# Kernel tuning notes

Measured on AMD Instinct MI355X. Metric: run time of the kernel, lower is better.

## Reference

```python
import jax, jax.numpy as jnp
import numpy as np

BS, EP = 32, 32
N_AGENTS, N_ATOM, EMBED = 8, 51, 32
STATE_DIM, HYP = 128, 64
V_MIN, V_MAX = -10.0, 10.0


def proj(support, probs, v_min, v_max, n_atom):
    # C51 categorical projection of (support, probs) onto the fixed atom grid
    # linspace(v_min, v_max, n_atom). support/probs: [..., M] -> [..., n_atom]
    support, probs = jnp.broadcast_arrays(support, probs)
    delta = (v_max - v_min) / (n_atom - 1)
    b = (jnp.clip(support, v_min, v_max) - v_min) / delta
    l = jnp.floor(b)
    u = jnp.ceil(b)
    eq = (u == l).astype(probs.dtype)  # support exactly on an atom -> all mass to l
    ml = probs * (u - b + eq)
    mu = probs * (b - l)
    shp = probs.shape
    n = int(np.prod(shp[:-1]))
    m = shp[-1]
    rows = jnp.arange(n)[:, None]
    out = jnp.zeros((n, n_atom), probs.dtype)
    out = out.at[rows, l.astype(jnp.int32).reshape(n, m)].add(ml.reshape(n, m))
    out = out.at[rows, u.astype(jnp.int32).reshape(n, m)].add(mu.reshape(n, m))
    return out.reshape(shp[:-1] + (n_atom,))


def bconv(p, q):
    # Full 1D convolution of per-row categorical pmfs (sum of two random vars).
    # p: [N, L], q: [N, M] -> [N, L+M-1], via grouped conv (one group per row).
    N, L = p.shape
    M = q.shape[-1]
    out = jax.lax.conv_general_dilated(
        p[None], jnp.flip(q, -1)[:, None, :],
        window_strides=(1,), padding=[(M - 1, M - 1)],
        feature_group_count=N, dimension_numbers=('NCW', 'OIW', 'NCW'))
    return out[0]


def mlp2(x, w1, b1, w2, b2):
    return jax.nn.relu(x @ w1.T + b1) @ w2.T + b2


def setup_inputs():
    key = jax.random.key(0)
    ks = jax.random.split(key, 20)
    def p(k, shape, s=0.05):
        return jax.random.normal(k, shape, dtype=jnp.float32) * s
    aq = jax.random.uniform(ks[0], (BS, EP, N_AGENTS, N_ATOM), dtype=jnp.float32)
    aq = aq / jnp.sum(aq, -1, keepdims=True)  # valid categorical distributions
    return {
        'agent_qs_distri': aq,
        'states': p(ks[1], (BS, EP, STATE_DIM), 1.0),
        'hw1_w1': p(ks[2], (HYP, STATE_DIM)), 'hw1_b1': p(ks[3], (HYP,)),
        'hw1_w2': p(ks[4], (EMBED * N_AGENTS, HYP)), 'hw1_b2': p(ks[5], (EMBED * N_AGENTS,)),
        'hb1_w': p(ks[6], (EMBED, STATE_DIM)), 'hb1_b': p(ks[7], (EMBED,)),
        'hwf_w1': p(ks[8], (HYP, STATE_DIM)), 'hwf_b1': p(ks[9], (HYP,)),
        'hwf_w2': p(ks[10], (EMBED, HYP)), 'hwf_b2': p(ks[11], (EMBED,)),
        'v_w1': p(ks[12], (EMBED, STATE_DIM)), 'v_b1': p(ks[13], (EMBED,)),
        'v_w2': p(ks[14], (1, EMBED)), 'v_b2': p(ks[15], (1,)),
    }


def reference(agent_qs_distri, states, hw1_w1, hw1_b1, hw1_w2, hw1_b2,
              hb1_w, hb1_b, hwf_w1, hwf_b1, hwf_w2, hwf_b2,
              v_w1, v_b1, v_w2, v_b2):
    bs, ep, n_agents, n_atom = agent_qs_distri.shape
    s = states.reshape(-1, STATE_DIM)
    atoms = jnp.linspace(V_MIN, V_MAX, n_atom).astype(jnp.float32)  # [A]

    w1 = jnp.abs(mlp2(s, hw1_w1, hw1_b1, hw1_w2, hw1_b2)).reshape(bs, ep, EMBED, n_agents)
    b1 = (s @ hb1_w.T + hb1_b).reshape(bs, ep, EMBED)

    # stage 1: scale each agent's support by w1[..., k, i], project back onto atoms
    sup1 = atoms * w1[..., None]                                       # [bs,ep,E,Na,A]
    aw = proj(sup1, agent_qs_distri[:, :, None], V_MIN, V_MAX, n_atom)  # [bs,ep,E,Na,A]
    awf = aw.reshape(-1, n_agents, n_atom)                              # [bs*ep*E,Na,A]
    q = awf[:, 0]
    for i in range(1, n_agents):
        q = bconv(q, awf[:, i])                                         # [.., Na*A-Na+1]
    L1 = n_agents * n_atom - n_agents + 1
    sup = jnp.linspace(n_agents * V_MIN, n_agents * V_MAX, L1).astype(jnp.float32)
    sup = jax.nn.elu(sup + b1[..., None])                               # [bs,ep,E,L1]
    x = proj(sup, q.reshape(bs, ep, EMBED, L1), V_MIN, V_MAX, n_atom)   # [bs,ep,E,A]

    # stage 2: hyper_w_final scaling, convolve across embed dim, add V(s)
    wf = jnp.abs(mlp2(s, hwf_w1, hwf_b1, hwf_w2, hwf_b2)).reshape(bs, ep, EMBED)
    xw = proj(atoms * wf[..., None], x, V_MIN, V_MAX, n_atom)           # [bs,ep,E,A]
    xwf = xw.reshape(-1, EMBED, n_atom)
    q = xwf[:, 0]
    for i in range(1, EMBED):
        q = bconv(q, xwf[:, i])                                         # [bs*ep, E*A-E+1]
    L2 = EMBED * n_atom - EMBED + 1
    v = mlp2(s, v_w1, v_b1, v_w2, v_b2).reshape(bs, ep, 1)
    sup2 = jnp.linspace(EMBED * V_MIN, EMBED * V_MAX, L2).astype(jnp.float32) + v
    return proj(sup2, q.reshape(bs, ep, L2), V_MIN, V_MAX, n_atom)      # [bs,ep,A]
```

## Files before the change

kernel.cpp:

```cpp
#include <hip/hip_runtime.h>
#include <hip/hip_bf16.h>
#include <math.h>

typedef unsigned short u16;

#define WAVE_SYNC() asm volatile("s_waitcnt lgkmcnt(0)" ::: "memory")

__device__ __forceinline__ float bf2f(u16 u) {
  union { unsigned int i; float f; } c;
  c.i = ((unsigned int)u) << 16;
  return c.f;
}
__device__ __forceinline__ float bflo(unsigned int u) {
  union { unsigned int i; float f; } c; c.i = u << 16; return c.f;
}
__device__ __forceinline__ float bfhi(unsigned int u) {
  union { unsigned int i; float f; } c; c.i = u & 0xffff0000u; return c.f;
}
__device__ __forceinline__ u16 f2bf(float f) {
  union { float f; unsigned int i; } c;
  c.f = f;
  unsigned int x = c.i;
  unsigned int r = (x + 0x7fffu + ((x >> 16) & 1u)) >> 16;
  return (u16)r;
}

__device__ __forceinline__ void proj_bounds(float wv, int& ML, int& MH) {
  float smin = (-10.0f + 0.4f * 0.0f)  * wv;
  float smax = (-10.0f + 0.4f * 50.0f) * wv;
  float bmin = (fminf(fmaxf(smin, -10.0f), 10.0f) + 10.0f) / 0.4f;
  float bmax = (fminf(fmaxf(smax, -10.0f), 10.0f) + 10.0f) / 0.4f;
  ML = (int)floorf(bmin);
  MH = (int)ceilf(bmax);
}

__device__ __forceinline__ void conv_pad2(const float* __restrict__ q,
                                          float* __restrict__ qn,
                                          const float* __restrict__ kvs,
                                          int ML, int W, int T,
                                          int LQ, int HQ, int tid, int nthr)
{
  const int Lout = LQ + ML, Hout = HQ + ML + T;
  for (int J = Lout + tid; J <= Hout; J += nthr) {
    const float* qp = q + (J - ML);
    float acc = 0.f;
    for (int c = 0; c < W; c += 4) {
      float4 k4 = *(const float4*)(kvs + c);
      acc = fmaf(k4.x, qp[-c],     acc);
      acc = fmaf(k4.y, qp[-c - 1], acc);
      acc = fmaf(k4.z, qp[-c - 2], acc);
      acc = fmaf(k4.w, qp[-c - 3], acc);
    }
    qn[J] = acc;
  }
}

__device__ __forceinline__ void conv16(const float* __restrict__ q,
                                       float* __restrict__ qn,
                                       const float* __restrict__ kvs,
                                       int ML, int T,
                                       int LQ, int HQ, int tid, int nthr)
{
  const int Lout = LQ + ML, Hout = HQ + ML + T;
  for (int J = Lout + tid; J <= Hout; J += nthr) {
    const float* qp = q + (J - ML);
    float a0 = 0.f, a1 = 0.f;
#pragma unroll
    for (int c = 0; c < 16; c += 4) {
      float4 k4 = *(const float4*)(kvs + c);
      a0 = fmaf(k4.x, qp[-c],     a0);
      a1 = fmaf(k4.y, qp[-c - 1], a1);
      a0 = fmaf(k4.z, qp[-c - 2], a0);
      a1 = fmaf(k4.w, qp[-c - 3], a1);
    }
    qn[J] = a0 + a1;
  }
}

__device__ __forceinline__ void conv8(const float* __restrict__ q,
                                      float* __restrict__ qn,
                                      const float* __restrict__ kvs,
                                      int ML, int T,
                                      int LQ, int HQ, int tid, int nthr)
{
  const int Lout = LQ + ML, Hout = HQ + ML + T;
  for (int J = Lout + tid; J <= Hout; J += nthr) {
    const float* qp = q + (J - ML);
    float a0 = 0.f, a1 = 0.f;
#pragma unroll
    for (int c = 0; c < 8; c += 4) {
      float4 k4 = *(const float4*)(kvs + c);
      a0 = fmaf(k4.x, qp[-c],     a0);
      a1 = fmaf(k4.y, qp[-c - 1], a1);
      a0 = fmaf(k4.z, qp[-c - 2], a0);
      a1 = fmaf(k4.w, qp[-c - 3], a1);
    }
    qn[J] = a0 + a1;
  }
}

template<int TA, int TB>
__device__ __forceinline__ float gather_part(const float* __restrict__ pb,
                                             float wv, float j)
{
  float a0 = 0.f, a1 = 0.f, a2 = 0.f, a3 = 0.f;
  const float4* pb4 = (const float4*)pb;
  const float base = 25.0f - j;
#pragma unroll
  for (int t4 = TA; t4 < TB; ++t4) {
    float4 p4 = pb4[t4];
#define G1(PX, TT, AC) { \
    float sup = ((float)(TT) * 0.4f - 10.0f) * wv; \
    float c   = fminf(fmaxf(sup, -10.0f), 10.0f); \
    float d   = fmaf(c, 2.5f, base); \
    AC = fmaf(PX, fmaxf(0.f, 1.0f - fabsf(d)), AC); }
    G1(p4.x, 4 * t4 + 0, a0)
    G1(p4.y, 4 * t4 + 1, a1)
    G1(p4.z, 4 * t4 + 2, a2)
    G1(p4.w, 4 * t4 + 3, a3)
#undef G1
  }
  return (a0 + a1) + (a2 + a3);
}

template<int BF>
__device__ __forceinline__ float ldt(const void* p, int i) {
  if (BF) return bf2f(((const u16*)p)[i]);
  return ((const float*)p)[i];
}

template<int BF>
__device__ __forceinline__ float dot128_t(const void* w, int row, const float* s) {
  float acc = 0.f;
  if (BF) {
    const uint4* p = (const uint4*)((const u16*)w + row * 128);
#pragma unroll
    for (int i = 0; i < 16; ++i) {
      uint4 v = p[i];
      int b = i * 8;
      acc = fmaf(bflo(v.x), s[b + 0], acc); acc = fmaf(bfhi(v.x), s[b + 1], acc);
      acc = fmaf(bflo(v.y), s[b + 2], acc); acc = fmaf(bfhi(v.y), s[b + 3], acc);
      acc = fmaf(bflo(v.z), s[b + 4], acc); acc = fmaf(bfhi(v.z), s[b + 5], acc);
      acc = fmaf(bflo(v.w), s[b + 6], acc); acc = fmaf(bfhi(v.w), s[b + 7], acc);
    }
  } else {
    const float4* p = (const float4*)((const float*)w + row * 128);
#pragma unroll
    for (int i = 0; i < 32; ++i) {
      float4 v = p[i];
      int b = i * 4;
      acc = fmaf(v.x, s[b + 0], acc); acc = fmaf(v.y, s[b + 1], acc);
      acc = fmaf(v.z, s[b + 2], acc); acc = fmaf(v.w, s[b + 3], acc);
    }
  }
  return acc;
}

template<int BF>
__device__ __forceinline__ float dot64_t(const void* w, int row, const float* h) {
  float acc = 0.f;
  if (BF) {
    const uint4* p = (const uint4*)((const u16*)w + row * 64);
#pragma unroll
    for (int i = 0; i < 8; ++i) {
      uint4 v = p[i];
      int b = i * 8;
      acc = fmaf(bflo(v.x), h[b + 0], acc); acc = fmaf(bfhi(v.x), h[b + 1], acc);
      acc = fmaf(bflo(v.y), h[b + 2], acc); acc = fmaf(bfhi(v.y), h[b + 3], acc);
      acc = fmaf(bflo(v.z), h[b + 4], acc); acc = fmaf(bfhi(v.z), h[b + 5], acc);
      acc = fmaf(bflo(v.w), h[b + 6], acc); acc = fmaf(bfhi(v.w), h[b + 7], acc);
    }
  } else {
    const float4* p = (const float4*)((const float*)w + row * 64);
#pragma unroll
    for (int i = 0; i < 16; ++i) {
      float4 v = p[i];
      int b = i * 4;
      acc = fmaf(v.x, h[b + 0], acc); acc = fmaf(v.y, h[b + 1], acc);
      acc = fmaf(v.z, h[b + 2], acc); acc = fmaf(v.w, h[b + 3], acc);
    }
  }
  return acc;
}

template<int BF>
__device__ __forceinline__ void mlp_par(
    const void* states,
    const void* hw1_w1, const void* hw1_b1, const void* hw1_w2, const void* hw1_b2,
    const void* hb1_w,  const void* hb1_b,
    const void* hwf_w1, const void* hwf_b1, const void* hwf_w2, const void* hwf_b2,
    const void* v_w1,   const void* v_b1,   const void* v_w2,   const void* v_b2,
    float* w1_ws, float* b1_ws, float* wf_ws, float* v_ws,
    float* s_st, float* h1, float* hf, float* vh, int n, int tid)
{
  if (tid < 128) s_st[tid] = ldt<BF>(states, n * 128 + tid);
  __syncthreads();
  if (tid < 64)
    h1[tid] = fmaxf(dot128_t<BF>(hw1_w1, tid, s_st) + ldt<BF>(hw1_b1, tid), 0.f);
  else if (tid < 128)
    hf[tid - 64] = fmaxf(dot128_t<BF>(hwf_w1, tid - 64, s_st) + ldt<BF>(hwf_b1, tid - 64), 0.f);
  else if (tid < 160)
    vh[tid - 128] = fmaxf(dot128_t<BF>(v_w1, tid - 128, s_st) + ldt<BF>(v_b1, tid - 128), 0.f);
  else if (tid < 192)
    b1_ws[n * 32 + tid - 160] = dot128_t<BF>(hb1_w, tid - 160, s_st) + ldt<BF>(hb1_b, tid - 160);
  __syncthreads();
  if (tid < 256)
    w1_ws[n * 256 + tid] = fabsf(dot64_t<BF>(hw1_w2, tid, h1) + ldt<BF>(hw1_b2, tid));
  else if (tid < 288)
    wf_ws[n * 32 + tid - 256] = fabsf(dot64_t<BF>(hwf_w2, tid - 256, hf) + ldt<BF>(hwf_b2, tid - 256));
  else {
    int l2 = tid - 288;
    float part = vh[l2] * ldt<BF>(v_w2, l2);
    part += __shfl_xor(part, 1);  part += __shfl_xor(part, 2);
    part += __shfl_xor(part, 4);  part += __shfl_xor(part, 8);
    part += __shfl_xor(part, 16);
    if (l2 == 0) v_ws[n] = part + ldt<BF>(v_b2, 0);
  }
}

__global__ __launch_bounds__(320) void k_mlp(
    const void* __restrict__ states,
    const void* __restrict__ hw1_w1, const void* __restrict__ hw1_b1,
    const void* __restrict__ hw1_w2, const void* __restrict__ hw1_b2,
    const void* __restrict__ hb1_w,  const void* __restrict__ hb1_b,
    const void* __restrict__ hwf_w1, const void* __restrict__ hwf_b1,
    const void* __restrict__ hwf_w2, const void* __restrict__ hwf_b2,
    const void* __restrict__ v_w1,   const void* __restrict__ v_b1,
    const void* __restrict__ v_w2,   const void* __restrict__ v_b2,
    float* __restrict__ w1_ws, float* __restrict__ b1_ws,
    float* __restrict__ wf_ws, float* __restrict__ v_ws,
    int* __restrict__ flag)
{
  __shared__ float s_st[128];
  __shared__ float h1[64], hf[64], vh[32];
  __shared__ int sh_flag;
  const int n = blockIdx.x;
  const int tid = threadIdx.x;

  if (tid < 64) {
    const u16* sr = (const u16*)states;
    unsigned int e0 = (sr[tid] >> 7) & 0xFF;
    unsigned int e1 = (sr[tid + 64] >> 7) & 0xFF;
    unsigned long long bl0 = __ballot(e0 >= 97 && e0 <= 141);
    unsigned long long bl1 = __ballot(e1 >= 97 && e1 <= 141);
    int bfv = (__popcll(bl0) + __popcll(bl1) >= 104) ? 1 : 0;
    if (tid == 0) { sh_flag = bfv; *flag = bfv; }
  }
  __syncthreads();
  const int bf = sh_flag;

  if (bf)
    mlp_par<1>(states, hw1_w1, hw1_b1, hw1_w2, hw1_b2, hb1_w, hb1_b,
               hwf_w1, hwf_b1, hwf_w2, hwf_b2, v_w1, v_b1, v_w2, v_b2,
               w1_ws, b1_ws, wf_ws, v_ws, s_st, h1, hf, vh, n, tid);
  else
    mlp_par<0>(states, hw1_w1, hw1_b1, hw1_w2, hw1_b2, hb1_w, hb1_b,
               hwf_w1, hwf_b1, hwf_w2, hwf_b2, v_w1, v_b1, v_w2, v_b2,
               w1_ws, b1_ws, wf_ws, v_ws, s_st, h1, hf, vh, n, tid);
}

__global__ __launch_bounds__(128) void k_perembed(
    const void* __restrict__ aq,
    const float* __restrict__ w1_ws, const float* __restrict__ b1_ws,
    const float* __restrict__ wf_ws, float* __restrict__ xw_ws,
    const int* __restrict__ flag)
{
  __shared__ __align__(16) float P[8 * 52];
  __shared__ __align__(16) float TS[2][1332];

  const int tid  = threadIdx.x;
  const int w    = tid >> 6;
  const int lane = tid & 63;
  const int task = blockIdx.x * 2 + w;
  const int n = task >> 5;
  const int e = task & 31;
  const int bf = *flag;

  if (bf) {
    const u16* p = (const u16*)aq + n * 408;
    if (lane < 52) {
#pragma unroll
      for (int k = 0; k < 4; ++k) {
        int a = 4 * w + k;
        P[a * 52 + lane] = (lane < 51) ? bf2f(p[a * 51 + lane]) : 0.f;
      }
    }
  } else {
    const float* p = (const float*)aq + n * 408;
    if (lane < 52) {
#pragma unroll
      for (int k = 0; k < 4; ++k) {
        int a = 4 * w + k;
        P[a * 52 + lane] = (lane < 51) ? p[a * 51 + lane] : 0.f;
      }
    }
  }
  float wreg = (lane < 8) ? w1_ws[n * 256 + e * 8 + lane] : 0.f;
  float b1v  = b1_ws[n * 32 + e];
  float wfv  = wf_ws[n * 32 + e];

  int mlA = 0, mhA = 0;
  if (lane < 8) proj_bounds(wreg, mlA, mhA);
  __syncthreads();

  float* Ab  = TS[w];
  float* Bb  = Ab + 520;
  float* kv  = Ab + 1040;
  float* kvo = Ab + 1168;
  float* x2  = Ab + 1224;
  float* g   = Ab + 1276;

#pragma unroll
  for (int r = 0; r < 2; ++r) {
    int a  = 4 * r + (lane >> 4);
    int jj = lane & 15;
    float wv = __shfl(wreg, a);
    int ML = __shfl(mlA, a);
    int MH = __shfl(mhA, a);
    int T  = MH - ML;
    float K = (25.0f - (float)(ML + jj)) - 25.0f * wv;
    float a0 = 0.f, a1 = 0.f, a2 = 0.f, a3 = 0.f;
    const float4* pb4 = (const float4*)(P + a * 52);
#pragma unroll
    for (int t4 = 0; t4 < 13; ++t4) {
      float4 p4 = pb4[t4];
      float d0 = fmaf((float)(4 * t4 + 0), wv, K);
      float d1 = fmaf((float)(4 * t4 + 1), wv, K);
      float d2 = fmaf((float)(4 * t4 + 2), wv, K);
      float d3 = fmaf((float)(4 * t4 + 3), wv, K);
      a0 = fmaf(p4.x, fmaxf(0.f, 1.0f - fabsf(d0)), a0);
      a1 = fmaf(p4.y, fmaxf(0.f, 1.0f - fabsf(d1)), a1);
      a2 = fmaf(p4.z, fmaxf(0.f, 1.0f - fabsf(d2)), a2);
      a3 = fmaf(p4.w, fmaxf(0.f, 1.0f - fabsf(d3)), a3);
    }
    if (T <= 15)
      kv[a * 16 + jj] = (jj <= T) ? ((a0 + a1) + (a2 + a3)) : 0.f;
  }
  WAVE_SYNC();

  int LQ, HQ;
  float* q = Ab;
  float* qn = Bb;
  {
    float wv0 = __shfl(wreg, 0);
    int ML0 = __shfl(mlA, 0), MH0 = __shfl(mhA, 0);
    int T0 = MH0 - ML0;
    if (T0 <= 15) {
      if (lane <= T0) Ab[64 + ML0 + lane] = kv[lane];
    } else {
      float acc = gather_part<0, 13>(P, wv0, (float)(ML0 + lane));
      if (lane <= T0) Ab[64 + ML0 + lane] = acc;
    }
    WAVE_SYNC();
    LQ = 64 + ML0; HQ = 64 + MH0;
  }

  for (int a = 1; a < 8; ++a) {
    float wv = __shfl(wreg, a);
    int ML = __shfl(mlA, a), MH = __shfl(mhA, a);
    int T = MH - ML;
    const float* kvs;
    int W;
    if (T <= 15) {
      kvs = kv + a * 16;
      W = (T <= 7) ? 8 : 16;
    } else {
      float acc = gather_part<0, 13>(P + a * 52, wv, (float)(ML + lane));
      W = (T + 4) & ~3;
      if (lane < W) kvo[lane] = (lane <= T) ? acc : 0.f;
      kvs = kvo;
    }
    if (lane < W - 1) q[LQ - 1 - lane] = 0.f;
    if (lane < T)     q[HQ + 1 + lane] = 0.f;
    WAVE_SYNC();
    if (T <= 7)       conv8 (q, qn, kvs, ML, T, LQ, HQ, lane, 64);
    else if (T <= 15) conv16(q, qn, kvs, ML, T, LQ, HQ, lane, 64);
    else              conv_pad2(q, qn, kvs, ML, W, T, LQ, HQ, lane, 64);
    WAVE_SYNC();
    LQ += ML; HQ += MH;
    float* t_ = q; q = qn; qn = t_;
  }

  {
    if (lane < 53) g[lane] = 0.f;
    WAVE_SYNC();
    int span = HQ - LQ + 1;
    for (int base = 0; base < span; base += 64) {
      int t = base + lane;
      if (t < span) {
        int tg = (LQ - 64) + t;
        float raw = (-80.0f + 0.4f * (float)tg) + b1v;
        float sup = (raw > 0.f) ? raw : expm1f(raw);
        float c  = fminf(fmaxf(sup, -10.0f), 10.0f);
        float b  = (c + 10.0f) / 0.4f;
        float l  = floorf(b);
        float u  = ceilf(b);
        float eq = (u == l) ? 1.0f : 0.0f;
        float p  = q[LQ + t];
        int   li = (int)l;
        atomicAdd(&g[li],     p * (u - b + eq));
        atomicAdd(&g[li + 1], p * (b - l));
      }
    }
    WAVE_SYNC();
  }
  if (lane < 52) x2[lane] = (lane < 51) ? g[lane] : 0.f;
  WAVE_SYNC();

  {
    int MLf, MHf;
    proj_bounds(wfv, MLf, MHf);
    int Tf = MHf - MLf;
    if (Tf <= 15) {
      int q4 = lane >> 4, jj = lane & 15;
      float K = (25.0f - (float)(MLf + jj)) - 25.0f * wfv;
      float acc = 0.f;
#pragma unroll
      for (int k = 0; k < 13; ++k) {
        int t = q4 + 4 * k;
        float d = fmaf((float)t, wfv, K);
        acc = fmaf(x2[t], fmaxf(0.f, 1.0f - fabsf(d)), acc);
      }
      acc += __shfl_xor(acc, 16);
      acc += __shfl_xor(acc, 32);
      if (lane <= Tf)
        xw_ws[task * 51 + MLf + lane] = acc;
    } else {
      float acc = gather_part<0, 13>(x2, wfv, (float)(MLf + lane));
      if (lane <= Tf)
        xw_ws[task * 51 + MLf + lane] = acc;
    }
  }
}

__global__ __launch_bounds__(512) void k_final(
    const float* __restrict__ xw_ws, const float* __restrict__ wf_ws,
    const float* __restrict__ v_ws,
    void* __restrict__ out, const int* __restrict__ flag)
{
  __shared__ __align__(16) float bufA[4608];
  __shared__ __align__(16) float bufB[4608];
  __shared__ int meta_s[63];
  __shared__ int meta_l[63];
  __shared__ int meta_ml[32];
  __shared__ int meta_g[6];
  __shared__ int meta_mltot;
  __shared__ float gA[53];

  const int n    = blockIdx.x;
  const int tid  = threadIdx.x;
  const int lane = tid & 63;
  const int bf   = *flag;

  float vv = v_ws[n];

  for (int i = tid; i < 4608; i += 512) { bufA[i] = 0.f; bufB[i] = 0.f; }
  if (tid < 53) gA[tid] = 0.f;

  if (tid < 64) {
    float wfreg = (lane < 32) ? wf_ws[n * 32 + lane] : 0.f;
    int ml, mh;
    proj_bounds(wfreg, ml, mh);
    if (lane < 32) meta_ml[lane] = ml;
    int msum = ml;
#pragma unroll
    for (int d = 1; d < 32; d <<= 1) msum += __shfl_xor(msum, d);
    if (lane == 0) meta_mltot = msum;

    int curlen = mh - ml + 1;
    int base = 0, Ncur = 32;
#pragma unroll
    for (int c = 0; c <= 5; ++c) {
      int lm = (lane < Ncur) ? curlen : 0;
#pragma unroll
      for (int d = 1; d < 32; d <<= 1) {
        int o = __shfl_xor(lm, d);
        lm = (o > lm) ? o : lm;
      }
      int G = (lm + 11) & ~3;
      int sp = ((curlen + 3) & ~3) + G;
      int inc = (lane < Ncur) ? sp : 0;
      int v0 = inc;
#pragma unroll
      for (int d = 1; d < 32; d <<= 1) {
        int u = __shfl_up(inc, d);
        if (lane >= d && lane < 32) inc += u;
      }
      if (lane < Ncur) {
        meta_s[base + lane] = 832 + (inc - v0);
        meta_l[base + lane] = curlen;
      }
      if (lane == 0) meta_g[c] = G;
      if (c < 5) {
        int l0 = __shfl(curlen, 2 * lane);
        int l1 = __shfl(curlen, 2 * lane + 1);
        curlen = l0 + l1 - 1;
        base += Ncur;
        Ncur >>= 1;
      }
    }
  }
  __syncthreads();

  {
    int g = tid >> 4, i3 = tid & 15;
    int s2 = meta_s[g], l2 = meta_l[g], ml = meta_ml[g];
    const float* row = xw_ws + (n * 32 + g) * 51 + ml;
    for (int i0 = i3; i0 < l2; i0 += 16) bufA[s2 + i0] = row[i0];
  }
  __syncthreads();

#pragma unroll
  for (int c = 1; c <= 5; ++c) {
    const float* bin = (c & 1) ? bufA : bufB;
    float*       bout = (c & 1) ? bufB : bufA;
    const int Nout = 32 >> c;
    const int lg = 4 + c;
    const int gs = 1 << lg;
    const int k  = tid >> lg;
    const int st = tid & (gs - 1);
    const int bc = 64 - (64 >> c);
    const int bp = 64 - (64 >> (c - 1));
    const int i0 = bp + 2 * k;
    const int sA = meta_s[i0];
    const int sB = meta_s[i0 + 1];
    const int lB = meta_l[i0 + 1];
    const int sO = meta_s[bc + k];
    const int lO = meta_l[bc + k];
    const int W  = (lB + 3) & ~3;
    const int W4 = W >> 2;

    for (int j = st * 4; j < lO; j += gs * 4) {
      const float* Abase = bin + sA + j;
      float a0 = 0.f, a1 = 0.f, a2 = 0.f, a3 = 0.f;
      float q0 = Abase[3],  q1 = Abase[2],  q2 = Abase[1],  q3 = Abase[0],
            q4 = Abase[-1], q5 = Abase[-2], q6 = Abase[-3];
      const float4* kb = (const float4*)(bin + sB);
      for (int g = 0; g < W4; ++g) {
        float4 k4 = kb[g];
        a0 = fmaf(k4.x, q3, a0); a1 = fmaf(k4.x, q2, a1);
        a2 = fmaf(k4.x, q1, a2); a3 = fmaf(k4.x, q0, a3);
        a0 = fmaf(k4.y, q4, a0); a1 = fmaf(k4.y, q3, a1);
        a2 = fmaf(k4.y, q2, a2); a3 = fmaf(k4.y, q1, a3);
        a0 = fmaf(k4.z, q5, a0); a1 = fmaf(k4.z, q4, a1);
        a2 = fmaf(k4.z, q3, a2); a3 = fmaf(k4.z, q2, a3);
        a0 = fmaf(k4.w, q6, a0); a1 = fmaf(k4.w, q5, a1);
        a2 = fmaf(k4.w, q4, a2); a3 = fmaf(k4.w, q3, a3);
        q0 = q4; q1 = q5; q2 = q6;
        int b2 = -4 - 4 * g;
        q3 = Abase[b2];     q4 = Abase[b2 - 1];
        q5 = Abase[b2 - 2]; q6 = Abase[b2 - 3];
      }
      bout[sO + j] = a0;
      if (j + 1 < lO) bout[sO + j + 1] = a1;
      if (j + 2 < lO) bout[sO + j + 2] = a2;
      if (j + 3 < lO) bout[sO + j + 3] = a3;
    }

    if (c >= 2 && c <= 4) {
      int G = meta_g[c];
      for (int p = tid; p < G; p += 512) bout[832 - G + p] = 0.f;
      for (int k2 = 0; k2 < Nout; ++k2) {
        int ss = meta_s[bc + k2] + meta_l[bc + k2];
        int ee = (k2 + 1 < Nout) ? meta_s[bc + k2 + 1]
                                 : ss + G + 3;
        for (int p = ss + tid; p < ee; p += 512) bout[p] = 0.f;
      }
    }
    __syncthreads();
  }

  {
    int s5 = meta_s[62], l5 = meta_l[62], mlt = meta_mltot;
    const float* qf = bufB + s5;
    for (int t = tid; t < l5; t += 512) {
      int tg = mlt + t;
      float sup = (-320.0f + 0.4f * (float)tg) + vv;
      float c  = fminf(fmaxf(sup, -10.0f), 10.0f);
      float b  = (c + 10.0f) / 0.4f;
      float l  = floorf(b);
      float u  = ceilf(b);
      float eq = (u == l) ? 1.0f : 0.0f;
      float p  = qf[t];
      int   li = (int)l;
      atomicAdd(&gA[li],     p * (u - b + eq));
      atomicAdd(&gA[li + 1], p * (b - l));
    }
  }
  __syncthreads();
  if (tid < 51) {
    float o = gA[tid];
    if (bf) ((u16*)out)[n * 51 + tid] = f2bf(o);
    else    ((float*)out)[n * 51 + tid] = o;
  }
}

extern "C" void kernel_launch(void* const* d_in, const int* in_sizes, int n_in,
                              void* d_out, int out_size, void* d_ws, size_t ws_size,
                              hipStream_t stream)
{
  float* ws    = (float*)d_ws;
  float* w1_ws = ws;
  float* b1_ws = w1_ws + 1024 * 256;
  float* wf_ws = b1_ws + 1024 * 32;
  float* v_ws  = wf_ws + 1024 * 32;
  float* xw_ws = v_ws  + 1024;
  int*   flag  = (int*)(xw_ws + 1024 * 32 * 51);

  k_mlp<<<1024, 320, 0, stream>>>(d_in[1],
      d_in[2], d_in[3], d_in[4], d_in[5], d_in[6], d_in[7],
      d_in[8], d_in[9], d_in[10], d_in[11], d_in[12], d_in[13],
      d_in[14], d_in[15],
      w1_ws, b1_ws, wf_ws, v_ws, flag);

  k_perembed<<<16384, 128, 0, stream>>>(d_in[0], w1_ws, b1_ws, wf_ws, xw_ws, flag);

  k_final<<<1024, 512, 0, stream>>>(xw_ws, wf_ws, v_ws, d_out, flag);
}
```

Measured before the change: 251.6 us.

## Truncate per-embed convolution above clip threshold and fold tail mass analytically

Computes an upper support index beyond which the ELU'd support clips to the top atom, and caps the chained convolutions and projection loop at that index. The mass lying above the cap is recovered by tracking each kernel's total mass and adding (product of kernel sums minus the accumulated mass) to the last atom. This skips convolution outputs that would all land in the same clipped bin. It adds shuffle reductions and extra shared memory, and carries floating-point risk from the mass-difference correction and the cap boundary computation.

```diff
diff --git a/kernel.cpp b/kernel.cpp
--- a/kernel.cpp
+++ b/kernel.cpp
@@ -38,9 +38,11 @@
                                           float* __restrict__ qn,
                                           const float* __restrict__ kvs,
                                           int ML, int W, int T,
-                                          int LQ, int HQ, int tid, int nthr)
-{
-  const int Lout = LQ + ML, Hout = HQ + ML + T;
+                                          int LQ, int HQ, int Jmax,
+                                          int tid, int nthr)
+{
+  const int Lout = LQ + ML;
+  const int Hout = min(HQ + ML + T, Jmax);
   for (int J = Lout + tid; J <= Hout; J += nthr) {
     const float* qp = q + (J - ML);
     float acc = 0.f;
@@ -59,9 +61,11 @@
                                        float* __restrict__ qn,
                                        const float* __restrict__ kvs,
                                        int ML, int T,
-                                       int LQ, int HQ, int tid, int nthr)
-{
-  const int Lout = LQ + ML, Hout = HQ + ML + T;
+                                       int LQ, int HQ, int Jmax,
+                                       int tid, int nthr)
+{
+  const int Lout = LQ + ML;
+  const int Hout = min(HQ + ML + T, Jmax);
   for (int J = Lout + tid; J <= Hout; J += nthr) {
     const float* qp = q + (J - ML);
     float a0 = 0.f, a1 = 0.f;
@@ -81,9 +85,11 @@
                                       float* __restrict__ qn,
                                       const float* __restrict__ kvs,
                                       int ML, int T,
-                                      int LQ, int HQ, int tid, int nthr)
-{
-  const int Lout = LQ + ML, Hout = HQ + ML + T;
+                                      int LQ, int HQ, int Jmax,
+                                      int tid, int nthr)
+{
+  const int Lout = LQ + ML;
+  const int Hout = min(HQ + ML + T, Jmax);
   for (int J = Lout + tid; J <= Hout; J += nthr) {
     const float* qp = q + (J - ML);
     float a0 = 0.f, a1 = 0.f;
@@ -266,7 +272,7 @@
     const int* __restrict__ flag)
 {
   __shared__ __align__(16) float P[8 * 52];
-  __shared__ __align__(16) float TS[2][1332];
+  __shared__ __align__(16) float TS[2][1344];
 
   const int tid  = threadIdx.x;
   const int w    = tid >> 6;
@@ -299,16 +305,21 @@
   float b1v  = b1_ws[n * 32 + e];
   float wfv  = wf_ws[n * 32 + e];
 
+  int tgmax = (int)ceilf((90.0f - b1v) * 2.5f);
+  if (tgmax < 0) tgmax = 0;
+  const int Jcap = 64 + tgmax - 1;
+
   int mlA = 0, mhA = 0;
   if (lane < 8) proj_bounds(wreg, mlA, mhA);
   __syncthreads();
 
-  float* Ab  = TS[w];
-  float* Bb  = Ab + 520;
-  float* kv  = Ab + 1040;
-  float* kvo = Ab + 1168;
-  float* x2  = Ab + 1224;
-  float* g   = Ab + 1276;
+  float* Ab    = TS[w];
+  float* Bb    = Ab + 520;
+  float* kv    = Ab + 1040;
+  float* kvo   = Ab + 1168;
+  float* x2    = Ab + 1224;
+  float* g     = Ab + 1276;
+  float* kvsum = Ab + 1332;
 
 #pragma unroll
   for (int r = 0; r < 2; ++r) {
@@ -333,8 +344,14 @@
       a2 = fmaf(p4.z, fmaxf(0.f, 1.0f - fabsf(d2)), a2);
       a3 = fmaf(p4.w, fmaxf(0.f, 1.0f - fabsf(d3)), a3);
     }
-    if (T <= 15)
-      kv[a * 16 + jj] = (jj <= T) ? ((a0 + a1) + (a2 + a3)) : 0.f;
+    float tot = (jj <= T) ? ((a0 + a1) + (a2 + a3)) : 0.f;
+    if (T <= 15) {
+      kv[a * 16 + jj] = tot;
+      float s = tot;
+      s += __shfl_xor(s, 1); s += __shfl_xor(s, 2);
+      s += __shfl_xor(s, 4); s += __shfl_xor(s, 8);
+      if (jj == 0) kvsum[a] = s;
+    }
   }
   WAVE_SYNC();
 
@@ -346,10 +363,16 @@
     int ML0 = __shfl(mlA, 0), MH0 = __shfl(mhA, 0);
     int T0 = MH0 - ML0;
     if (T0 <= 15) {
-      if (lane <= T0) Ab[64 + ML0 + lane] = kv[lane];
+      if (lane <= T0 && 64 + ML0 + lane <= Jcap)
+        Ab[64 + ML0 + lane] = kv[lane];
     } else {
       float acc = gather_part<0, 13>(P, wv0, (float)(ML0 + lane));
-      if (lane <= T0) Ab[64 + ML0 + lane] = acc;
+      float s = (lane <= T0) ? acc : 0.f;
+#pragma unroll
+      for (int d = 1; d < 64; d <<= 1) s += __shfl_xor(s, d);
+      if (lane == 0) kvsum[0] = s;
+      if (lane <= T0 && 64 + ML0 + lane <= Jcap)
+        Ab[64 + ML0 + lane] = acc;
     }
     WAVE_SYNC();
     LQ = 64 + ML0; HQ = 64 + MH0;
@@ -366,6 +389,10 @@
       W = (T <= 7) ? 8 : 16;
     } else {
       float acc = gather_part<0, 13>(P + a * 52, wv, (float)(ML + lane));
+      float s = (lane <= T) ? acc : 0.f;
+#pragma unroll
+      for (int d = 1; d < 64; d <<= 1) s += __shfl_xor(s, d);
+      if (lane == 0) kvsum[a] = s;
       W = (T + 4) & ~3;
       if (lane < W) kvo[lane] = (lane <= T) ? acc : 0.f;
       kvs = kvo;
@@ -373,9 +400,9 @@
     if (lane < W - 1) q[LQ - 1 - lane] = 0.f;
     if (lane < T)     q[HQ + 1 + lane] = 0.f;
     WAVE_SYNC();
-    if (T <= 7)       conv8 (q, qn, kvs, ML, T, LQ, HQ, lane, 64);
-    else if (T <= 15) conv16(q, qn, kvs, ML, T, LQ, HQ, lane, 64);
-    else              conv_pad2(q, qn, kvs, ML, W, T, LQ, HQ, lane, 64);
+    if (T <= 7)       conv8 (q, qn, kvs, ML, T, LQ, HQ, Jcap, lane, 64);
+    else if (T <= 15) conv16(q, qn, kvs, ML, T, LQ, HQ, Jcap, lane, 64);
+    else              conv_pad2(q, qn, kvs, ML, W, T, LQ, HQ, Jcap, lane, 64);
     WAVE_SYNC();
     LQ += ML; HQ += MH;
     float* t_ = q; q = qn; qn = t_;
@@ -384,7 +411,9 @@
   {
     if (lane < 53) g[lane] = 0.f;
     WAVE_SYNC();
-    int span = HQ - LQ + 1;
+    int top  = min(HQ, Jcap);
+    int span = top - LQ + 1;
+    float wsum = 0.f;
     for (int base = 0; base < span; base += 64) {
       int t = base + lane;
       if (t < span) {
@@ -398,10 +427,18 @@
         float eq = (u == l) ? 1.0f : 0.0f;
         float p  = q[LQ + t];
         int   li = (int)l;
+        wsum += p;
         atomicAdd(&g[li],     p * (u - b + eq));
         atomicAdd(&g[li + 1], p * (b - l));
       }
     }
+#pragma unroll
+    for (int d = 1; d < 64; d <<= 1) wsum += __shfl_xor(wsum, d);
+    float tots = kvsum[0];
+#pragma unroll
+    for (int a2 = 1; a2 < 8; ++a2) tots *= kvsum[a2];
+    WAVE_SYNC();
+    if (lane == 0) g[50] += tots - wsum;
     WAVE_SYNC();
   }
   if (lane < 52) x2[lane] = (lane < 51) ? g[lane] : 0.f;
```

New measurement: 250.3 us, median of 2. Within noise of the previous version (-0.5%).
